# Kernel optimization log

Hardware: AMD Instinct MI355X
Metric: run time of the kernel (lower is better)

Reference implementation:

```python
import jax, jax.numpy as jnp
import numpy as np

B, T, H, W = 1, 8, 48, 48
EMBED, HEADS = 512, 8
HD = EMBED // HEADS          # 64
KS = 3                       # spatial neighborhood kernel
ROT = HD // 3                # 21 -> 2*(21//2)=20 rotary dims per axis, 60 total
MAX_FREQ = 256.0
EPS = 1e-6


def _rms_norm(x, w):
    return x * jax.lax.rsqrt(jnp.mean(x * x, axis=-1, keepdims=True) + EPS) * w


def _axis_freqs(L, base):
    # freqs_for='pixel': positions in [-1, 1], freqs = linspace(1, max_freq/2)*pi
    pos = jnp.linspace(-1.0, 1.0, L)
    f = pos[:, None] * base[None, :]          # (L, ROT//2)
    return jnp.repeat(f, 2, axis=-1)          # (L, 2*(ROT//2)) interleaved pairs


def _axial_freqs(t, h, w):
    base = jnp.linspace(1.0, MAX_FREQ / 2.0, ROT // 2) * jnp.pi
    ft, fh, fw = _axis_freqs(t, base), _axis_freqs(h, base), _axis_freqs(w, base)
    d = ft.shape[-1]
    ft = jnp.broadcast_to(ft[:, None, None, :], (t, h, w, d))
    fh = jnp.broadcast_to(fh[None, :, None, :], (t, h, w, d))
    fw = jnp.broadcast_to(fw[None, None, :, :], (t, h, w, d))
    return jnp.concatenate([ft, fh, fw], axis=-1)  # (t, h, w, 3*d)


def _rotate_half(x):
    x1, x2 = x[..., ::2], x[..., 1::2]
    return jnp.stack((-x2, x1), axis=-1).reshape(x.shape)


def _apply_rope(freqs, x):
    r = freqs.shape[-1]
    xr, xt = x[..., :r], x[..., r:]
    xr = xr * jnp.cos(freqs) + _rotate_half(xr) * jnp.sin(freqs)
    return jnp.concatenate([xr, xt], axis=-1)


def reference(x, w_qkv, w_out, qnorm_w, knorm_w):
    b, t, h, w, c = x.shape
    # fused QKV: per-head contiguous [q|k|v] chunk of size 3*HD (matches
    # rearrange '(heads head_dim)' with head_dim = 3*HD, then tensor_split(3, -1))
    qkv = (x @ w_qkv.T).reshape(b, t, h, w, HEADS, 3 * HD)
    q, k, v = qkv[..., :HD], qkv[..., HD:2 * HD], qkv[..., 2 * HD:]
    q = _rms_norm(q, qnorm_w)
    k = _rms_norm(k, knorm_w)
    freqs = _axial_freqs(t, h, w)[:, :, :, None, :]  # broadcast over heads
    q = _apply_rope(freqs, q)
    k = _apply_rope(freqs, k)
    # neighborhood attention: full along t, clamped KSxKS window over (h, w)
    ih = jnp.clip(jnp.arange(h) - KS // 2, 0, h - KS)[:, None] + jnp.arange(KS)
    iw = jnp.clip(jnp.arange(w) - KS // 2, 0, w - KS)[:, None] + jnp.arange(KS)
    IH = ih[:, :, None, None]  # (h, KS, 1, 1)
    IW = iw[None, None, :, :]  # (1, 1, w, KS)
    kw = k[:, :, IH, IW]       # (b, t, h, KS, w, KS, heads, HD)
    vw = v[:, :, IH, IW]
    scores = jnp.einsum('btxynd,bsxiyjnd->bntxysij', q, kw) * (HD ** -0.5)
    attn = jax.nn.softmax(scores.reshape(b, HEADS, t, h, w, -1), axis=-1)
    attn = attn.reshape(scores.shape)
    out = jnp.einsum('bntxysij,bsxiyjnd->btxynd', attn, vw)
    out = out.reshape(b, t, h, w, c)
    return out @ w_out.T


def setup_inputs():
    key = jax.random.key(0)
    k1, k2, k3 = jax.random.split(key, 3)
    x = jax.random.normal(k1, (B, T, H, W, EMBED), jnp.float32)
    w_qkv = jax.random.normal(k2, (3 * EMBED, EMBED), jnp.float32) * 0.02
    w_out = jax.random.normal(k3, (EMBED, EMBED), jnp.float32) * 0.02
    qnorm_w = jnp.ones((HD,), jnp.float32)
    knorm_w = jnp.ones((HD,), jnp.float32)
    return dict(x=x, w_qkv=w_qkv, w_out=w_out, qnorm_w=qnorm_w, knorm_w=knorm_w)
```

## Files before the change

### kernel.cpp

```cpp
#include <hip/hip_runtime.h>
#include <hip/hip_bf16.h>
#include <math.h>

#define TOK 18432
#define EMB 512
#define NH 8
#define HD_ 64
#define HH 48
#define WW 48

typedef __attribute__((ext_vector_type(8))) __bf16 bf16x8;
typedef __attribute__((ext_vector_type(4))) float  f32x4;
typedef __attribute__((ext_vector_type(8))) unsigned short u16x8;

__device__ __forceinline__ ushort f2bf(float x) {
    __hip_bfloat16 b = __float2bfloat16(x);
    return *(ushort*)&b;
}
__device__ __forceinline__ float bf2f(ushort u) {
    __hip_bfloat16 b = *(__hip_bfloat16*)&u;
    return __bfloat162float(b);
}

__device__ __forceinline__ void gload16(const void* g, void* l) {
    __builtin_amdgcn_global_load_lds((const __attribute__((address_space(1))) void*)g,
                                     (__attribute__((address_space(3))) void*)l,
                                     16, 0, 0);
}

__device__ __forceinline__ f32x4 mfma_bf16(bf16x8 a, bf16x8 b, f32x4 c) {
    return __builtin_amdgcn_mfma_f32_16x16x32_bf16(a, b, c, 0, 0, 0);
}

__global__ __launch_bounds__(256) void init_misc(const float* __restrict__ x,
                                                 ushort* __restrict__ xhi,
                                                 const float* __restrict__ wq,
                                                 ushort* __restrict__ wqhi,
                                                 const float* __restrict__ wo,
                                                 ushort* __restrict__ wohi,
                                                 float2* __restrict__ tabs) {
    int b = blockIdx.x;
    if (b < 10240) {
        const float* src;
        ushort* dst;
        int i;
        if (b < 9216)      { src = x;  dst = xhi;  i = b * 256 + threadIdx.x; }
        else if (b < 9984) { src = wq; dst = wqhi; i = (b - 9216) * 256 + threadIdx.x; }
        else               { src = wo; dst = wohi; i = (b - 9984) * 256 + threadIdx.x; }
        float4 v = ((const float4*)src)[i];
        ushort4 h = {f2bf(v.x), f2bf(v.y), f2bf(v.z), f2bf(v.w)};
        ((ushort4*)dst)[i] = h;
    } else {
        int idx = (b - 10240) * 256 + threadIdx.x;
        if (idx >= 104 * 10) return;
        int row = idx / 10, j = idx % 10;
        float base = fmaf((float)j, 127.0f / 9.0f, 1.0f) * 3.14159265358979323846f;
        float pos;
        if (row < 8)       pos = fmaf((float)row,        2.0f / 7.0f,  -1.0f);
        else if (row < 56) pos = fmaf((float)(row - 8),  2.0f / 47.0f, -1.0f);
        else               pos = fmaf((float)(row - 56), 2.0f / 47.0f, -1.0f);
        float f = pos * base;
        tabs[idx] = make_float2(cosf(f), sinf(f));
    }
}

__global__ __launch_bounds__(256) void gemm_qkv(const ushort* __restrict__ Ah,
                                                const ushort* __restrict__ Bh,
                                                const float2* __restrict__ tabs,
                                                const float* __restrict__ qnw,
                                                const float* __restrict__ knw,
                                                ushort* __restrict__ qbf,
                                                ushort* __restrict__ kbf,
                                                ushort* __restrict__ vbf) {
    const int K = 512, nM = 12;
    __shared__ __align__(16) char smem[49152];
#define AS_(b) ((ushort*)(smem + (b) * 16384))
#define BS_(b) ((ushort*)(smem + (b) * 16384 + 8192))
    int nwg = gridDim.x;
    int bid = blockIdx.x;
    int cpx = nwg >> 3;
    int swz = (bid & 7) * cpx + (bid >> 3);
    int bm = (swz % nM) * 128, bn = (swz / nM) * 128;
    int tid = threadIdx.x;
    int lane = tid & 63, wave = tid >> 6;
    int wr = wave >> 1, wc = wave & 1;
    int fr = lane & 15, kg = lane >> 4;

    f32x4 acc[4][4];
#pragma unroll
    for (int m = 0; m < 4; ++m)
#pragma unroll
        for (int n = 0; n < 4; ++n) acc[m][n] = (f32x4){0.f, 0.f, 0.f, 0.f};

    auto stage = [&](int buf, int k0) {
#pragma unroll
        for (int it = 0; it < 2; ++it) {
            int f = it * 256 + tid;
            int row = f >> 2, ch = f & 3;
            int sl = ch ^ ((row >> 1) & 3);
            gload16(Ah + (size_t)(bm + row) * K + k0 + sl * 8, AS_(buf) + f * 8);
            gload16(Bh + (size_t)(bn + row) * K + k0 + sl * 8, BS_(buf) + f * 8);
        }
    };

    int nt = K >> 5;
    stage(0, 0);
    int cb = 0, nb = 1;
    int ksw = (kg ^ ((fr >> 1) & 3)) * 8;
    for (int t = 0; t < nt; ++t) {
        if (t + 1 < nt) {
            stage(nb, (t + 1) << 5);
            asm volatile("s_waitcnt vmcnt(4)" ::: "memory");
        } else {
            asm volatile("s_waitcnt vmcnt(0)" ::: "memory");
        }
        __builtin_amdgcn_s_barrier();
        __builtin_amdgcn_sched_barrier(0);
        const ushort* Bc = BS_(cb);
        const ushort* Ac = AS_(cb);
        bf16x8 bh[4];
#pragma unroll
        for (int n = 0; n < 4; ++n)
            bh[n] = *(const bf16x8*)&Bc[(wc * 64 + n * 16 + fr) * 32 + ksw];
#pragma unroll
        for (int m = 0; m < 4; ++m) {
            bf16x8 ah = *(const bf16x8*)&Ac[(wr * 64 + m * 16 + fr) * 32 + ksw];
#pragma unroll
            for (int n = 0; n < 4; ++n)
                acc[m][n] = mfma_bf16(ah, bh[n], acc[m][n]);
        }
        cb = (cb + 1 == 3) ? 0 : cb + 1;
        nb = (nb + 1 == 3) ? 0 : nb + 1;
    }
    __syncthreads();

    int g = (bm >> 6) + wr;
    int type = g % 3;
    int h = g / 3;
    ushort* obuf = (type == 0) ? qbf : (type == 1) ? kbf : vbf;
    float qsc = (type == 0) ? 0.125f : 1.0f;
    float4 wv[4];
    if (type < 2) {
        const float* wptr = type ? knw : qnw;
#pragma unroll
        for (int m = 0; m < 4; ++m)
            wv[m] = *(const float4*)&wptr[m * 16 + kg * 4];
    }
    char* tb = smem + wave * 5120;
    size_t obase = (size_t)h * TOK + bn + wc * 64;

#pragma unroll
    for (int hp = 0; hp < 2; ++hp) {
#pragma unroll
        for (int nn = 0; nn < 2; ++nn) {
            int n = hp * 2 + nn;
            int tk = bn + wc * 64 + n * 16 + fr;
            if (type == 2) {
#pragma unroll
                for (int m = 0; m < 4; ++m) {
                    ushort4 pk = {f2bf(acc[m][n][0]), f2bf(acc[m][n][1]),
                                  f2bf(acc[m][n][2]), f2bf(acc[m][n][3])};
                    *(ushort4*)(tb + (nn * 16 + fr) * 160 + (m * 16 + kg * 4) * 2) = pk;
                }
            } else {
                float s = 0.f;
#pragma unroll
                for (int m = 0; m < 4; ++m)
#pragma unroll
                    for (int i = 0; i < 4; ++i)
                        s = fmaf(acc[m][n][i], acc[m][n][i], s);
                s += __shfl_xor(s, 16);
                s += __shfl_xor(s, 32);
                float inv = rsqrtf(s * (1.0f / 64.0f) + 1e-6f);
                int t = tk / (HH * WW);
                int rem = tk % (HH * WW);
                int xx = rem / WW, yy = rem % WW;
#pragma unroll
                for (int m = 0; m < 4; ++m) {
                    float r[4];
                    const float* wm = (const float*)&wv[m];
#pragma unroll
                    for (int u = 0; u < 2; ++u) {
                        int dc0 = m * 16 + kg * 4 + 2 * u;
                        float xn0 = acc[m][n][2 * u]     * inv * wm[2 * u];
                        float xn1 = acc[m][n][2 * u + 1] * inv * wm[2 * u + 1];
                        if (dc0 < 60) {
                            int p = dc0 >> 1;
                            int tr = (p < 10) ? t * 10 + p
                                   : (p < 20) ? (8 + xx) * 10 + (p - 10)
                                              : (56 + yy) * 10 + (p - 20);
                            float2 cs = tabs[tr];
                            r[2 * u]     = fmaf(xn0, cs.x, -xn1 * cs.y);
                            r[2 * u + 1] = fmaf(xn1, cs.x,  xn0 * cs.y);
                        } else {
                            r[2 * u] = xn0;
                            r[2 * u + 1] = xn1;
                        }
                    }
                    ushort4 pk = {f2bf(r[0] * qsc), f2bf(r[1] * qsc),
                                  f2bf(r[2] * qsc), f2bf(r[3] * qsc)};
                    *(ushort4*)(tb + (nn * 16 + fr) * 160 + (m * 16 + kg * 4) * 2) = pk;
                }
            }
        }
#pragma unroll
        for (int j = 0; j < 4; ++j) {
            int row = j * 8 + (lane >> 3);
            int c16 = (lane & 7) * 16;
            u16x8 v = *(const u16x8*)(tb + row * 160 + c16);
            size_t tok = obase + hp * 32 + row;
            *(u16x8*)(obuf + tok * 64 + (lane & 7) * 8) = v;
        }
    }
#undef AS_
#undef BS_
}

__global__ __launch_bounds__(256) void gemm_out(const ushort* __restrict__ Ah,
                                                const ushort* __restrict__ Bh,
                                                float* __restrict__ C) {
    const int N = 512, K = 512, nbx = 4;
    __shared__ __align__(16) char smem[49152];
#define AS_(b) ((ushort*)(smem + (b) * 16384))
#define BS_(b) ((ushort*)(smem + (b) * 16384 + 8192))
    int nwg = gridDim.x;
    int bid = blockIdx.x;
    int cpx = nwg >> 3;
    int swz = (bid & 7) * cpx + (bid >> 3);
    int bm = (swz / nbx) * 128, bn = (swz % nbx) * 128;
    int tid = threadIdx.x;
    int lane = tid & 63, wave = tid >> 6;
    int wr = wave >> 1, wc = wave & 1;
    int fr = lane & 15, kg = lane >> 4;

    f32x4 acc[4][4];
#pragma unroll
    for (int m = 0; m < 4; ++m)
#pragma unroll
        for (int n = 0; n < 4; ++n) acc[m][n] = (f32x4){0.f, 0.f, 0.f, 0.f};

    auto stage = [&](int buf, int k0) {
#pragma unroll
        for (int it = 0; it < 2; ++it) {
            int f = it * 256 + tid;
            int row = f >> 2, ch = f & 3;
            int sl = ch ^ ((row >> 1) & 3);
            gload16(Ah + (size_t)(bm + row) * K + k0 + sl * 8, AS_(buf) + f * 8);
            gload16(Bh + (size_t)(bn + row) * K + k0 + sl * 8, BS_(buf) + f * 8);
        }
    };

    int nt = K >> 5;
    stage(0, 0);
    int cb = 0, nb = 1;
    int ksw = (kg ^ ((fr >> 1) & 3)) * 8;
    for (int t = 0; t < nt; ++t) {
        if (t + 1 < nt) {
            stage(nb, (t + 1) << 5);
            asm volatile("s_waitcnt vmcnt(4)" ::: "memory");
        } else {
            asm volatile("s_waitcnt vmcnt(0)" ::: "memory");
        }
        __builtin_amdgcn_s_barrier();
        __builtin_amdgcn_sched_barrier(0);
        const ushort* Bc = BS_(cb);
        const ushort* Ac = AS_(cb);
        bf16x8 bh[4];
#pragma unroll
        for (int n = 0; n < 4; ++n)
            bh[n] = *(const bf16x8*)&Bc[(wc * 64 + n * 16 + fr) * 32 + ksw];
#pragma unroll
        for (int m = 0; m < 4; ++m) {
            bf16x8 ah = *(const bf16x8*)&Ac[(wr * 64 + m * 16 + fr) * 32 + ksw];
#pragma unroll
            for (int n = 0; n < 4; ++n)
                acc[m][n] = mfma_bf16(ah, bh[n], acc[m][n]);
        }
        cb = (cb + 1 == 3) ? 0 : cb + 1;
        nb = (nb + 1 == 3) ? 0 : nb + 1;
    }
#pragma unroll
    for (int m = 0; m < 4; ++m) {
        int row0 = bm + wr * 64 + m * 16 + kg * 4;
#pragma unroll
        for (int n = 0; n < 4; ++n) {
            int col = bn + wc * 64 + n * 16 + fr;
#pragma unroll
            for (int i = 0; i < 4; ++i)
                C[(size_t)(row0 + i) * N + col] = acc[m][n][i];
        }
    }
#undef AS_
#undef BS_
}

__global__ __launch_bounds__(256) void attn_mfma(const ushort* __restrict__ qbf,
                                                 const ushort* __restrict__ kbf,
                                                 const ushort* __restrict__ vbf,
                                                 ushort* __restrict__ ohi) {
    __shared__ __align__(16) char smem[45568];
    constexpr int Q_OFF = 0;
    constexpr int K_OFF = 4096;
    constexpr int V_OFF = 20480;
    constexpr int P_OFF = 36864;
    constexpr int XM_OFF = 45056;
    constexpr int XS_OFF = 45312;

    int patch = blockIdx.x, head = blockIdx.y;
    int bi = patch / 24, bj = patch % 24;
    int x0 = bi * 2, y0 = bj * 2;
    int ubx = min(max(x0 - 1, 0), 44), uby = min(max(y0 - 1, 0), 44);
    int tid = threadIdx.x, lane = tid & 63, w = tid >> 6;
    int fr = lane & 15, kg = lane >> 4;
    size_t hbase = (size_t)head * TOK;

    {
        int f = tid;
        int row = f >> 3, sp = f & 7, sl = sp ^ (row & 7);
        int t = row >> 2, px = (row >> 1) & 1, py = row & 1;
        size_t tok = ((size_t)(t * HH + x0 + px)) * WW + (y0 + py);
        gload16(qbf + (hbase + tok) * 64 + sl * 8, smem + Q_OFF + f * 16);
    }
#pragma unroll
    for (int it = 0; it < 4; ++it) {
        int f = it * 256 + tid;
        int row = f >> 3, sp = f & 7, sl = sp ^ (row & 7);
        int s = row >> 4, ki = (row >> 2) & 3, kj = row & 3;
        size_t tok = ((size_t)(s * HH + ubx + ki)) * WW + (uby + kj);
        gload16(kbf + (hbase + tok) * 64 + sl * 8, smem + K_OFF + f * 16);
    }
#pragma unroll
    for (int it = 0; it < 2; ++it) {
        int u = it * 256 + tid;
        int sk = u >> 4, dg = u & 15;
        int s = sk >> 2, ki = sk & 3;
        ushort4 rv[4];
#pragma unroll
        for (int kj = 0; kj < 4; ++kj) {
            size_t tok = ((size_t)(s * HH + ubx + ki)) * WW + (uby + kj);
            rv[kj] = *(const ushort4*)(vbf + (hbase + tok) * 64 + dg * 4);
        }
        const ushort* rr = (const ushort*)rv;
#pragma unroll
        for (int dd = 0; dd < 4; ++dd) {
            int d = dg * 4 + dd;
            ushort4 val = {rr[dd], rr[4 + dd], rr[8 + dd], rr[12 + dd]};
            *(ushort4*)(smem + V_OFF + d * 256 + ((sk * 8) ^ ((d & 7) << 4))) = val;
        }
    }
    __syncthreads();

    float* XM = (float*)(smem + XM_OFF);
    float* XS = (float*)(smem + XS_OFF);
    int qt = w & 1, mh = w >> 1;
    int q = qt * 16 + fr;
    {
        bf16x8 qb[2];
#pragma unroll
        for (int ks = 0; ks < 2; ++ks)
            qb[ks] = *(const bf16x8*)(smem + Q_OFF + q * 128 +
                                      ((ks * 64 + kg * 16) ^ ((fr & 7) << 4)));
        f32x4 sc[4];
#pragma unroll
        for (int mm = 0; mm < 4; ++mm) sc[mm] = (f32x4){0.f, 0.f, 0.f, 0.f};
        __builtin_amdgcn_s_setprio(1);
#pragma unroll
        for (int mm = 0; mm < 4; ++mm) {
            int m = mh * 4 + mm;
#pragma unroll
            for (int ks = 0; ks < 2; ++ks) {
                bf16x8 a = *(const bf16x8*)(smem + K_OFF + (m * 16 + fr) * 128 +
                                            ((ks * 64 + kg * 16) ^ ((fr & 7) << 4)));
                sc[mm] = mfma_bf16(a, qb[ks], sc[mm]);
            }
        }
        __builtin_amdgcn_s_setprio(0);
        int xq = x0 + ((q >> 1) & 1), yq = y0 + (q & 1);
        int lox = min(max(xq - 1, 0), 45) - ubx;
        int loy = min(max(yq - 1, 0), 45) - uby;
        bool vki = ((unsigned)(kg - lox)) <= 2u;
        float mx = -1e30f;
        if (vki) {
#pragma unroll
            for (int mm = 0; mm < 4; ++mm)
#pragma unroll
                for (int i = 0; i < 4; ++i)
                    if (((unsigned)(i - loy)) <= 2u) mx = fmaxf(mx, sc[mm][i]);
        }
        mx = fmaxf(mx, __shfl_xor(mx, 16));
        mx = fmaxf(mx, __shfl_xor(mx, 32));
        if (kg == 0) XM[(qt * 2 + mh) * 16 + fr] = mx;
        __syncthreads();
        mx = fmaxf(XM[(qt * 2 + 0) * 16 + fr], XM[(qt * 2 + 1) * 16 + fr]);
        float sum = 0.f;
#pragma unroll
        for (int mm = 0; mm < 4; ++mm)
#pragma unroll
            for (int i = 0; i < 4; ++i) {
                bool v = vki && (((unsigned)(i - loy)) <= 2u);
                float e = v ? __expf(sc[mm][i] - mx) : 0.f;
                sc[mm][i] = e;
                sum += e;
            }
        sum += __shfl_xor(sum, 16);
        sum += __shfl_xor(sum, 32);
        if (kg == 0) XS[(qt * 2 + mh) * 16 + fr] = sum;
        __syncthreads();
        float inv = 1.0f / (XS[(qt * 2 + 0) * 16 + fr] + XS[(qt * 2 + 1) * 16 + fr]);
#pragma unroll
        for (int mm = 0; mm < 4; ++mm) {
            int m = mh * 4 + mm;
            ushort4 pk = {f2bf(sc[mm][0] * inv), f2bf(sc[mm][1] * inv),
                          f2bf(sc[mm][2] * inv), f2bf(sc[mm][3] * inv)};
            *(ushort4*)(smem + P_OFF + q * 256 +
                        ((m * 32 + kg * 8) ^ ((q & 7) << 4))) = pk;
        }
    }
    __syncthreads();

    f32x4 ov[2];
    ov[0] = (f32x4){0.f, 0.f, 0.f, 0.f};
    ov[1] = (f32x4){0.f, 0.f, 0.f, 0.f};
    __builtin_amdgcn_s_setprio(1);
#pragma unroll
    for (int kb = 0; kb < 4; ++kb) {
        bf16x8 a = *(const bf16x8*)(smem + V_OFF + (w * 16 + fr) * 256 +
                                    ((kb * 64 + kg * 16) ^ ((fr & 7) << 4)));
#pragma unroll
        for (int nt2 = 0; nt2 < 2; ++nt2) {
            bf16x8 b = *(const bf16x8*)(smem + P_OFF + (nt2 * 16 + fr) * 256 +
                                        ((kb * 64 + kg * 16) ^ ((fr & 7) << 4)));
            ov[nt2] = mfma_bf16(a, b, ov[nt2]);
        }
    }
    __builtin_amdgcn_s_setprio(0);
#pragma unroll
    for (int nt2 = 0; nt2 < 2; ++nt2) {
        int qq = nt2 * 16 + fr;
        int t = qq >> 2, px = (qq >> 1) & 1, py = qq & 1;
        size_t tok = ((size_t)(t * HH + x0 + px)) * WW + (y0 + py);
        size_t ob = tok * 512 + head * 64 + w * 16 + kg * 4;
        ushort4 hv = {f2bf(ov[nt2][0]), f2bf(ov[nt2][1]),
                      f2bf(ov[nt2][2]), f2bf(ov[nt2][3])};
        *(ushort4*)&ohi[ob] = hv;
    }
}

extern "C" void kernel_launch(void* const* d_in, const int* in_sizes, int n_in,
                              void* d_out, int out_size, void* d_ws, size_t ws_size,
                              hipStream_t stream) {
    const float* x     = (const float*)d_in[0];
    const float* w_qkv = (const float*)d_in[1];
    const float* w_out = (const float*)d_in[2];
    const float* qnw   = (const float*)d_in[3];
    const float* knw   = (const float*)d_in[4];
    float* out = (float*)d_out;
    char*  ws  = (char*)d_ws;

    const size_t TABS_B = 16384;
    const size_t WQ_B   = (size_t)1536 * 512 * 2;
    const size_t WO_B   = (size_t)512 * 512 * 2;

    float2* tabs = (float2*)ws;
    ushort* wqhi = (ushort*)(ws + TABS_B);
    ushort* wohi = wqhi + (size_t)1536 * 512;
    ushort* qbf  = (ushort*)(ws + TABS_B + WQ_B + WO_B);
    ushort* kbf  = qbf + (size_t)TOK * 512;
    ushort* vbf  = kbf + (size_t)TOK * 512;
    ushort* ohi  = vbf + (size_t)TOK * 512;

    ushort* xhi = (ushort*)d_out;

    init_misc<<<10245, 256, 0, stream>>>(x, xhi, w_qkv, wqhi, w_out, wohi, tabs);

    gemm_qkv<<<(1536 / 128) * (TOK / 128), 256, 0, stream>>>(
        wqhi, xhi, tabs, qnw, knw, qbf, kbf, vbf);
    attn_mfma<<<dim3(576, NH), 256, 0, stream>>>(qbf, kbf, vbf, ohi);
    gemm_out<<<(TOK / 128) * (512 / 128), 256, 0, stream>>>(ohi, wohi, out);
}
```

Before: 103.0 us.

## Use 8 waves per block in QKV and output GEMMs

Both GEMM kernels now run with 512 threads (8 waves) instead of 256. Each wave covers a 64x32 sub-tile rather than 64x64, and each thread issues one staged global-to-LDS load per operand per k-step, so the wait count drops from 4 to 2. The aim is more waves resident per CU to hide latency, with fewer accumulator registers per wave. The cost is more LDS A-fragment reads per MFMA (less register reuse of B) and more barrier participants. In gemm_qkv the per-wave epilogue scratch region (wave*5120) now extends to 40 KB of the 48 KB shared buffer.

```diff
diff --git a/kernel.cpp b/kernel.cpp
--- a/kernel.cpp
+++ b/kernel.cpp
@@ -64,7 +64,7 @@
     }
 }
 
-__global__ __launch_bounds__(256) void gemm_qkv(const ushort* __restrict__ Ah,
+__global__ __launch_bounds__(512) void gemm_qkv(const ushort* __restrict__ Ah,
                                                 const ushort* __restrict__ Bh,
                                                 const float2* __restrict__ tabs,
                                                 const float* __restrict__ qnw,
@@ -83,24 +83,20 @@
     int bm = (swz % nM) * 128, bn = (swz / nM) * 128;
     int tid = threadIdx.x;
     int lane = tid & 63, wave = tid >> 6;
-    int wr = wave >> 1, wc = wave & 1;
+    int wr = wave >> 2, wc = wave & 3;
     int fr = lane & 15, kg = lane >> 4;
 
-    f32x4 acc[4][4];
+    f32x4 acc[4][2];
 #pragma unroll
     for (int m = 0; m < 4; ++m)
 #pragma unroll
-        for (int n = 0; n < 4; ++n) acc[m][n] = (f32x4){0.f, 0.f, 0.f, 0.f};
+        for (int n = 0; n < 2; ++n) acc[m][n] = (f32x4){0.f, 0.f, 0.f, 0.f};
 
     auto stage = [&](int buf, int k0) {
-#pragma unroll
-        for (int it = 0; it < 2; ++it) {
-            int f = it * 256 + tid;
-            int row = f >> 2, ch = f & 3;
-            int sl = ch ^ ((row >> 1) & 3);
-            gload16(Ah + (size_t)(bm + row) * K + k0 + sl * 8, AS_(buf) + f * 8);
-            gload16(Bh + (size_t)(bn + row) * K + k0 + sl * 8, BS_(buf) + f * 8);
-        }
+        int row = tid >> 2, ch = tid & 3;
+        int sl = ch ^ ((row >> 1) & 3);
+        gload16(Ah + (size_t)(bm + row) * K + k0 + sl * 8, AS_(buf) + tid * 8);
+        gload16(Bh + (size_t)(bn + row) * K + k0 + sl * 8, BS_(buf) + tid * 8);
     };
 
     int nt = K >> 5;
@@ -110,7 +106,7 @@
     for (int t = 0; t < nt; ++t) {
         if (t + 1 < nt) {
             stage(nb, (t + 1) << 5);
-            asm volatile("s_waitcnt vmcnt(4)" ::: "memory");
+            asm volatile("s_waitcnt vmcnt(2)" ::: "memory");
         } else {
             asm volatile("s_waitcnt vmcnt(0)" ::: "memory");
         }
@@ -118,15 +114,15 @@
         __builtin_amdgcn_sched_barrier(0);
         const ushort* Bc = BS_(cb);
         const ushort* Ac = AS_(cb);
-        bf16x8 bh[4];
-#pragma unroll
-        for (int n = 0; n < 4; ++n)
-            bh[n] = *(const bf16x8*)&Bc[(wc * 64 + n * 16 + fr) * 32 + ksw];
+        bf16x8 bh[2];
+#pragma unroll
+        for (int n = 0; n < 2; ++n)
+            bh[n] = *(const bf16x8*)&Bc[(wc * 32 + n * 16 + fr) * 32 + ksw];
 #pragma unroll
         for (int m = 0; m < 4; ++m) {
             bf16x8 ah = *(const bf16x8*)&Ac[(wr * 64 + m * 16 + fr) * 32 + ksw];
 #pragma unroll
-            for (int n = 0; n < 4; ++n)
+            for (int n = 0; n < 2; ++n)
                 acc[m][n] = mfma_bf16(ah, bh[n], acc[m][n]);
         }
         cb = (cb + 1 == 3) ? 0 : cb + 1;
@@ -147,76 +143,72 @@
             wv[m] = *(const float4*)&wptr[m * 16 + kg * 4];
     }
     char* tb = smem + wave * 5120;
-    size_t obase = (size_t)h * TOK + bn + wc * 64;
-
-#pragma unroll
-    for (int hp = 0; hp < 2; ++hp) {
-#pragma unroll
-        for (int nn = 0; nn < 2; ++nn) {
-            int n = hp * 2 + nn;
-            int tk = bn + wc * 64 + n * 16 + fr;
-            if (type == 2) {
-#pragma unroll
-                for (int m = 0; m < 4; ++m) {
-                    ushort4 pk = {f2bf(acc[m][n][0]), f2bf(acc[m][n][1]),
-                                  f2bf(acc[m][n][2]), f2bf(acc[m][n][3])};
-                    *(ushort4*)(tb + (nn * 16 + fr) * 160 + (m * 16 + kg * 4) * 2) = pk;
+    size_t obase = (size_t)h * TOK + bn + wc * 32;
+
+#pragma unroll
+    for (int n = 0; n < 2; ++n) {
+        int tk = bn + wc * 32 + n * 16 + fr;
+        if (type == 2) {
+#pragma unroll
+            for (int m = 0; m < 4; ++m) {
+                ushort4 pk = {f2bf(acc[m][n][0]), f2bf(acc[m][n][1]),
+                              f2bf(acc[m][n][2]), f2bf(acc[m][n][3])};
+                *(ushort4*)(tb + (n * 16 + fr) * 160 + (m * 16 + kg * 4) * 2) = pk;
+            }
+        } else {
+            float s = 0.f;
+#pragma unroll
+            for (int m = 0; m < 4; ++m)
+#pragma unroll
+                for (int i = 0; i < 4; ++i)
+                    s = fmaf(acc[m][n][i], acc[m][n][i], s);
+            s += __shfl_xor(s, 16);
+            s += __shfl_xor(s, 32);
+            float inv = rsqrtf(s * (1.0f / 64.0f) + 1e-6f);
+            int t = tk / (HH * WW);
+            int rem = tk % (HH * WW);
+            int xx = rem / WW, yy = rem % WW;
+#pragma unroll
+            for (int m = 0; m < 4; ++m) {
+                float r[4];
+                const float* wm = (const float*)&wv[m];
+#pragma unroll
+                for (int u = 0; u < 2; ++u) {
+                    int dc0 = m * 16 + kg * 4 + 2 * u;
+                    float xn0 = acc[m][n][2 * u]     * inv * wm[2 * u];
+                    float xn1 = acc[m][n][2 * u + 1] * inv * wm[2 * u + 1];
+                    if (dc0 < 60) {
+                        int p = dc0 >> 1;
+                        int tr = (p < 10) ? t * 10 + p
+                               : (p < 20) ? (8 + xx) * 10 + (p - 10)
+                                          : (56 + yy) * 10 + (p - 20);
+                        float2 cs = tabs[tr];
+                        r[2 * u]     = fmaf(xn0, cs.x, -xn1 * cs.y);
+                        r[2 * u + 1] = fmaf(xn1, cs.x,  xn0 * cs.y);
+                    } else {
+                        r[2 * u] = xn0;
+                        r[2 * u + 1] = xn1;
+                    }
                 }
-            } else {
-                float s = 0.f;
-#pragma unroll
-                for (int m = 0; m < 4; ++m)
-#pragma unroll
-                    for (int i = 0; i < 4; ++i)
-                        s = fmaf(acc[m][n][i], acc[m][n][i], s);
-                s += __shfl_xor(s, 16);
-                s += __shfl_xor(s, 32);
-                float inv = rsqrtf(s * (1.0f / 64.0f) + 1e-6f);
-                int t = tk / (HH * WW);
-                int rem = tk % (HH * WW);
-                int xx = rem / WW, yy = rem % WW;
-#pragma unroll
-                for (int m = 0; m < 4; ++m) {
-                    float r[4];
-                    const float* wm = (const float*)&wv[m];
-#pragma unroll
-                    for (int u = 0; u < 2; ++u) {
-                        int dc0 = m * 16 + kg * 4 + 2 * u;
-                        float xn0 = acc[m][n][2 * u]     * inv * wm[2 * u];
-                        float xn1 = acc[m][n][2 * u + 1] * inv * wm[2 * u + 1];
-                        if (dc0 < 60) {
-                            int p = dc0 >> 1;
-                            int tr = (p < 10) ? t * 10 + p
-                                   : (p < 20) ? (8 + xx) * 10 + (p - 10)
-                                              : (56 + yy) * 10 + (p - 20);
-                            float2 cs = tabs[tr];
-                            r[2 * u]     = fmaf(xn0, cs.x, -xn1 * cs.y);
-                            r[2 * u + 1] = fmaf(xn1, cs.x,  xn0 * cs.y);
-                        } else {
-                            r[2 * u] = xn0;
-                            r[2 * u + 1] = xn1;
-                        }
-                    }
-                    ushort4 pk = {f2bf(r[0] * qsc), f2bf(r[1] * qsc),
-                                  f2bf(r[2] * qsc), f2bf(r[3] * qsc)};
-                    *(ushort4*)(tb + (nn * 16 + fr) * 160 + (m * 16 + kg * 4) * 2) = pk;
-                }
+                ushort4 pk = {f2bf(r[0] * qsc), f2bf(r[1] * qsc),
+                              f2bf(r[2] * qsc), f2bf(r[3] * qsc)};
+                *(ushort4*)(tb + (n * 16 + fr) * 160 + (m * 16 + kg * 4) * 2) = pk;
             }
         }
-#pragma unroll
-        for (int j = 0; j < 4; ++j) {
-            int row = j * 8 + (lane >> 3);
-            int c16 = (lane & 7) * 16;
-            u16x8 v = *(const u16x8*)(tb + row * 160 + c16);
-            size_t tok = obase + hp * 32 + row;
-            *(u16x8*)(obuf + tok * 64 + (lane & 7) * 8) = v;
-        }
+    }
+#pragma unroll
+    for (int j = 0; j < 4; ++j) {
+        int row = j * 8 + (lane >> 3);
+        int c16 = (lane & 7) * 16;
+        u16x8 v = *(const u16x8*)(tb + row * 160 + c16);
+        size_t tok = obase + row;
+        *(u16x8*)(obuf + tok * 64 + (lane & 7) * 8) = v;
     }
 #undef AS_
 #undef BS_
 }
 
-__global__ __launch_bounds__(256) void gemm_out(const ushort* __restrict__ Ah,
+__global__ __launch_bounds__(512) void gemm_out(const ushort* __restrict__ Ah,
                                                 const ushort* __restrict__ Bh,
                                                 float* __restrict__ C) {
     const int N = 512, K = 512, nbx = 4;
@@ -230,24 +222,20 @@
     int bm = (swz / nbx) * 128, bn = (swz % nbx) * 128;
     int tid = threadIdx.x;
     int lane = tid & 63, wave = tid >> 6;
-    int wr = wave >> 1, wc = wave & 1;
+    int wr = wave >> 2, wc = wave & 3;
     int fr = lane & 15, kg = lane >> 4;
 
-    f32x4 acc[4][4];
+    f32x4 acc[4][2];
 #pragma unroll
     for (int m = 0; m < 4; ++m)
 #pragma unroll
-        for (int n = 0; n < 4; ++n) acc[m][n] = (f32x4){0.f, 0.f, 0.f, 0.f};
+        for (int n = 0; n < 2; ++n) acc[m][n] = (f32x4){0.f, 0.f, 0.f, 0.f};
 
     auto stage = [&](int buf, int k0) {
-#pragma unroll
-        for (int it = 0; it < 2; ++it) {
-            int f = it * 256 + tid;
-            int row = f >> 2, ch = f & 3;
-            int sl = ch ^ ((row >> 1) & 3);
-            gload16(Ah + (size_t)(bm + row) * K + k0 + sl * 8, AS_(buf) + f * 8);
-            gload16(Bh + (size_t)(bn + row) * K + k0 + sl * 8, BS_(buf) + f * 8);
-        }
+        int row = tid >> 2, ch = tid & 3;
+        int sl = ch ^ ((row >> 1) & 3);
+        gload16(Ah + (size_t)(bm + row) * K + k0 + sl * 8, AS_(buf) + tid * 8);
+        gload16(Bh + (size_t)(bn + row) * K + k0 + sl * 8, BS_(buf) + tid * 8);
     };
 
     int nt = K >> 5;
@@ -257,7 +245,7 @@
     for (int t = 0; t < nt; ++t) {
         if (t + 1 < nt) {
             stage(nb, (t + 1) << 5);
-            asm volatile("s_waitcnt vmcnt(4)" ::: "memory");
+            asm volatile("s_waitcnt vmcnt(2)" ::: "memory");
         } else {
             asm volatile("s_waitcnt vmcnt(0)" ::: "memory");
         }
@@ -265,15 +253,15 @@
         __builtin_amdgcn_sched_barrier(0);
         const ushort* Bc = BS_(cb);
         const ushort* Ac = AS_(cb);
-        bf16x8 bh[4];
-#pragma unroll
-        for (int n = 0; n < 4; ++n)
-            bh[n] = *(const bf16x8*)&Bc[(wc * 64 + n * 16 + fr) * 32 + ksw];
+        bf16x8 bh[2];
+#pragma unroll
+        for (int n = 0; n < 2; ++n)
+            bh[n] = *(const bf16x8*)&Bc[(wc * 32 + n * 16 + fr) * 32 + ksw];
 #pragma unroll
         for (int m = 0; m < 4; ++m) {
             bf16x8 ah = *(const bf16x8*)&Ac[(wr * 64 + m * 16 + fr) * 32 + ksw];
 #pragma unroll
-            for (int n = 0; n < 4; ++n)
+            for (int n = 0; n < 2; ++n)
                 acc[m][n] = mfma_bf16(ah, bh[n], acc[m][n]);
         }
         cb = (cb + 1 == 3) ? 0 : cb + 1;
@@ -283,8 +271,8 @@
     for (int m = 0; m < 4; ++m) {
         int row0 = bm + wr * 64 + m * 16 + kg * 4;
 #pragma unroll
-        for (int n = 0; n < 4; ++n) {
-            int col = bn + wc * 64 + n * 16 + fr;
+        for (int n = 0; n < 2; ++n) {
+            int col = bn + wc * 32 + n * 16 + fr;
 #pragma unroll
             for (int i = 0; i < 4; ++i)
                 C[(size_t)(row0 + i) * N + col] = acc[m][n][i];
@@ -473,8 +461,8 @@
 
     init_misc<<<10245, 256, 0, stream>>>(x, xhi, w_qkv, wqhi, w_out, wohi, tabs);
 
-    gemm_qkv<<<(1536 / 128) * (TOK / 128), 256, 0, stream>>>(
+    gemm_qkv<<<(1536 / 128) * (TOK / 128), 512, 0, stream>>>(
         wqhi, xhi, tabs, qnw, knw, qbf, kbf, vbf);
     attn_mfma<<<dim3(576, NH), 256, 0, stream>>>(qbf, kbf, vbf, ohi);
-    gemm_out<<<(TOK / 128) * (512 / 128), 256, 0, stream>>>(ohi, wohi, out);
-}
+    gemm_out<<<(TOK / 128) * (512 / 128), 512, 0, stream>>>(ohi, wohi, out);
+}
```

After: 101.2 us. No clear change (-1.7%).
